# Optimization experiments

Hardware: AMD Instinct MI355X
Metric: run time of the kernel (lower is better)

Reference implementation:

```python
import jax, jax.numpy as jnp
import numpy as np
from jax import lax

THRESH = 1.0
MIN_VMEM = -1.0

def _conv(x, w, stride):
    # x: [N,C,H,W], w: [O,I,kh,kw]
    return lax.conv_general_dilated(
        x, w, window_strides=(stride, stride), padding=((1, 1), (1, 1)),
        dimension_numbers=("NCHW", "OIHW", "NCHW"))

def _avgpool2(x):
    n, c, h, w = x.shape
    return x.reshape(n, c, h // 2, 2, w // 2, 2).mean(axis=(3, 5))

def _iaf(x_bt, B, T):
    # x_bt: [B*T, ...] -> sinabs IAFSqueeze: reshape to [B,T,...], scan over T.
    feat = x_bt.shape[1:]
    seq = x_bt.reshape((B, T) + feat)
    seq_t = jnp.moveaxis(seq, 1, 0)  # [T, B, ...]

    def step(v, u):
        v = v + u                              # integrate
        s = (v >= THRESH).astype(v.dtype)      # SingleSpike
        v = v * (1.0 - s)                      # MembraneReset -> 0
        v = jnp.maximum(v, MIN_VMEM)           # min_v_mem clamp
        return v, s

    v0 = jnp.zeros(seq_t.shape[1:], dtype=x_bt.dtype)
    _, spikes = lax.scan(step, v0, seq_t)      # spikes: [T, B, ...]
    return jnp.moveaxis(spikes, 0, 1).reshape((B * T,) + feat)

def setup_inputs() -> dict:
    key = jax.random.key(0)
    k0, k1, k2, k3, k4 = jax.random.split(key, 5)
    x = jax.random.normal(k0, (25, 40, 2, 128, 128), jnp.float32)
    w1 = jax.random.normal(k1, (8, 2, 3, 3), jnp.float32) * 0.3
    w2 = jax.random.normal(k2, (16, 8, 3, 3), jnp.float32) * 0.2
    w3 = jax.random.normal(k3, (64, 1024), jnp.float32) * 0.1
    w4 = jax.random.normal(k4, (11, 64), jnp.float32) * 0.2
    return {"x": x, "w1": w1, "w2": w2, "w3": w3, "w4": w4}

def reference(x, w1, w2, w3, w4):
    B, T, C, H, W = x.shape
    h = x.reshape(B * T, C, H, W)
    h = _conv(h, w1, 2)          # [BT, 8, 64, 64]
    h = _iaf(h, B, T)
    h = _avgpool2(h)             # [BT, 8, 32, 32]
    h = _conv(h, w2, 2)          # [BT, 16, 16, 16]
    h = _iaf(h, B, T)
    h = _avgpool2(h)             # [BT, 16, 8, 8]
    h = h.reshape(B * T, -1)     # [BT, 1024]
    h = h @ w3.T                 # [BT, 64]
    h = _iaf(h, B, T)
    h = h @ w4.T                 # [BT, 11]
    h = _iaf(h, B, T)
    return h.reshape(B, T, -1)
```

## Files before the change

kernel.cpp:

```cpp
#include <hip/hip_runtime.h>

#define THRESH 1.0f
#define MIN_VMEM -1.0f

__device__ __forceinline__ float iaf_step(float& v, float u) {
    v += u;
    float s = (v >= THRESH) ? 1.f : 0.f;
    v = (s > 0.f) ? 0.f : v;
    v = fmaxf(v, MIN_VMEM);
    return s;
}

__global__ __launch_bounds__(64) void k1_conv1_iaf_pool(
        const float* __restrict__ x, const float* __restrict__ w1,
        float* __restrict__ ws1) {
    const int lane = threadIdx.x;
    const int q = blockIdx.x >> 1;
    const int g = blockIdx.x & 1;
    const int b = blockIdx.y;
    const bool q0 = (q == 0);

    float w[4][18];
    #pragma unroll
    for (int j = 0; j < 4; j++)
        #pragma unroll
        for (int k = 0; k < 18; k++)
            w[j][k] = w1[(4 * g + j) * 18 + k];

    const int iy0 = 4 * q - 1;
    int ro[5];
    #pragma unroll
    for (int r = 0; r < 5; r++) ro[r] = max(iy0 + r, 0) * 128;
    const float* xb = x + (size_t)(b * 40) * 32768 + 2 * lane;

    float2 A[10], Bv[10], N0[10], N1[10];
    #pragma unroll
    for (int ci = 0; ci < 2; ci++)
        #pragma unroll
        for (int r = 0; r < 5; r++) {
            A[ci * 5 + r]  = *(const float2*)(xb + ci * 16384 + ro[r]);
            Bv[ci * 5 + r] = *(const float2*)(xb + 32768 + ci * 16384 + ro[r]);
        }
    if (q0) {
        A[0] = make_float2(0.f, 0.f);  A[5] = make_float2(0.f, 0.f);
        Bv[0] = make_float2(0.f, 0.f); Bv[5] = make_float2(0.f, 0.f);
    }

    float vA[4], vB[4];
    #pragma unroll
    for (int j = 0; j < 4; j++) { vA[j] = 0.f; vB[j] = 0.f; }

    for (int tt = 0; tt < 20; tt++) {
        if (tt < 19) {
            const float* xn = xb + (size_t)(2 * tt + 2) * 32768;
            #pragma unroll
            for (int ci = 0; ci < 2; ci++)
                #pragma unroll
                for (int r = 0; r < 5; r++) {
                    N0[ci * 5 + r] = *(const float2*)(xn + ci * 16384 + ro[r]);
                    N1[ci * 5 + r] = *(const float2*)(xn + 32768 + ci * 16384 + ro[r]);
                }
        }
        #pragma unroll
        for (int half = 0; half < 2; half++) {
            const float2* F = half ? Bv : A;
            const int t = 2 * tt + half;
            float xm[10];
            #pragma unroll
            for (int r = 0; r < 10; r++) {
                const float up = __shfl_up(F[r].y, 1);
                xm[r] = (lane == 0) ? 0.f : up;
            }
            float preA[4], preB[4];
            #pragma unroll
            for (int j = 0; j < 4; j++) { preA[j] = 0.f; preB[j] = 0.f; }
            #pragma unroll
            for (int ci = 0; ci < 2; ci++)
                #pragma unroll
                for (int ky = 0; ky < 3; ky++) {
                    const int rA = ci * 5 + ky;
                    const int rB = rA + 2;
                    #pragma unroll
                    for (int j = 0; j < 4; j++) {
                        const float w0 = w[j][ci * 9 + ky * 3 + 0];
                        const float w1v = w[j][ci * 9 + ky * 3 + 1];
                        const float w2v = w[j][ci * 9 + ky * 3 + 2];
                        preA[j] += xm[rA] * w0 + F[rA].x * w1v + F[rA].y * w2v;
                        preB[j] += xm[rB] * w0 + F[rB].x * w1v + F[rB].y * w2v;
                    }
                }
            const size_t nbase = ((size_t)(b * 40 + t) * 8 + 4 * g) * 1024 + q * 32;
            #pragma unroll
            for (int j = 0; j < 4; j++) {
                float s = iaf_step(vA[j], preA[j]) + iaf_step(vB[j], preB[j]);
                s += __shfl_down(s, 1);
                if (!(lane & 1))
                    ws1[nbase + (size_t)j * 1024 + (lane >> 1)] = s * 0.25f;
            }
        }
        if (q0) {
            N0[0] = make_float2(0.f, 0.f); N0[5] = make_float2(0.f, 0.f);
            N1[0] = make_float2(0.f, 0.f); N1[5] = make_float2(0.f, 0.f);
        }
        #pragma unroll
        for (int r = 0; r < 10; r++) { A[r] = N0[r]; Bv[r] = N1[r]; }
    }
}

#define K2_CIS 1224

__global__ __launch_bounds__(256) void k2a_conv2(
        const float* __restrict__ ws1, const float* __restrict__ w2,
        float* __restrict__ u2) {
    __shared__ float F[8 * K2_CIS];
    const int n = blockIdx.x;
    const int tid = threadIdx.x;

    for (int i = tid; i < 8 * K2_CIS; i += 256) F[i] = 0.f;
    __syncthreads();
    const float4* src = (const float4*)(ws1 + (size_t)n * 8192);
    #pragma unroll
    for (int k = 0; k < 8; k++) {
        const int i = tid + 256 * k;
        const float4 q = src[i];
        const int ci = i >> 8;
        const int rr = i & 255;
        const int r = rr >> 3, c4 = rr & 7;
        float* d = &F[ci * K2_CIS + (r + 1) * 36 + 1 + 4 * c4];
        d[0] = q.x; d[1] = q.y; d[2] = q.z; d[3] = q.w;
    }
    __syncthreads();

    const int wv = tid >> 6;
    const int ln = tid & 63;
    const int oy = ln >> 2;
    const int ox4 = ln & 3;

    float acc[4][4];
    #pragma unroll
    for (int j = 0; j < 4; j++)
        #pragma unroll
        for (int k = 0; k < 4; k++) acc[j][k] = 0.f;

    #pragma unroll
    for (int ci = 0; ci < 8; ci++) {
        float q[3][9];
        const int base = ci * K2_CIS + (2 * oy) * 36 + 8 * ox4;
        #pragma unroll
        for (int ky = 0; ky < 3; ky++) {
            const float4 qa = *(const float4*)&F[base + ky * 36];
            const float4 qb = *(const float4*)&F[base + ky * 36 + 4];
            q[ky][0] = qa.x; q[ky][1] = qa.y; q[ky][2] = qa.z; q[ky][3] = qa.w;
            q[ky][4] = qb.x; q[ky][5] = qb.y; q[ky][6] = qb.z; q[ky][7] = qb.w;
            q[ky][8] = F[base + ky * 36 + 8];
        }
        #pragma unroll
        for (int j = 0; j < 4; j++) {
            const int co_u = __builtin_amdgcn_readfirstlane(4 * wv + j);
            const float* wb = w2 + co_u * 72 + ci * 9;
            float wm[9];
            #pragma unroll
            for (int m = 0; m < 9; m++) wm[m] = wb[m];
            #pragma unroll
            for (int k = 0; k < 4; k++)
                #pragma unroll
                for (int ky = 0; ky < 3; ky++)
                    #pragma unroll
                    for (int kx = 0; kx < 3; kx++)
                        acc[j][k] += q[ky][2 * k + kx] * wm[ky * 3 + kx];
        }
    }
    float* db = u2 + (size_t)n * 4096 + oy * 16 + 4 * ox4;
    #pragma unroll
    for (int j = 0; j < 4; j++) {
        const int co = 4 * wv + j;
        *(float4*)(db + co * 256) =
            make_float4(acc[j][0], acc[j][1], acc[j][2], acc[j][3]);
    }
}

__global__ __launch_bounds__(64) void k2b_scan(
        const float* __restrict__ u2, float* __restrict__ ws2) {
    const int id = blockIdx.x * 64 + threadIdx.x;
    const int b = id >> 10;
    const int c = (id >> 6) & 15;
    const int pp = id & 63;
    const int py = pp >> 3, px = pp & 7;
    const float* base = u2 + (size_t)(b * 40) * 4096 + c * 256
                      + (2 * py) * 16 + 2 * px;
    float* ob = ws2 + (size_t)(b * 40) * 1024 + c * 64 + py * 8 + px;

    float v0 = 0.f, v1 = 0.f, v2 = 0.f, v3 = 0.f;
    float2 P[2][8][2];
    #pragma unroll
    for (int tt = 0; tt < 8; tt++) {
        const float* nb = base + (size_t)tt * 4096;
        P[0][tt][0] = *(const float2*)(nb);
        P[0][tt][1] = *(const float2*)(nb + 16);
    }
    #pragma unroll
    for (int bt = 0; bt < 5; bt++) {
        if (bt < 4) {
            #pragma unroll
            for (int tt = 0; tt < 8; tt++) {
                const float* nb = base + (size_t)(8 * (bt + 1) + tt) * 4096;
                P[(bt + 1) & 1][tt][0] = *(const float2*)(nb);
                P[(bt + 1) & 1][tt][1] = *(const float2*)(nb + 16);
            }
        }
        #pragma unroll
        for (int tt = 0; tt < 8; tt++) {
            const float2 b0 = P[bt & 1][tt][0];
            const float2 b1 = P[bt & 1][tt][1];
            const float s = iaf_step(v0, b0.x) + iaf_step(v1, b0.y)
                          + iaf_step(v2, b1.x) + iaf_step(v3, b1.y);
            ob[(size_t)(8 * bt + tt) * 1024] = s * 0.25f;
        }
    }
}

__global__ __launch_bounds__(256) void k3_fc1(
        const float* __restrict__ ws2, const float* __restrict__ w3,
        float* __restrict__ ws3) {
    __shared__ float rows[2048];
    const int n0 = blockIdx.x * 2;
    const int tid = threadIdx.x;
    const float4* s = (const float4*)(ws2 + (size_t)n0 * 1024);
    #pragma unroll
    for (int k = 0; k < 2; k++)
        ((float4*)rows)[tid + 256 * k] = s[tid + 256 * k];
    __syncthreads();
    const int o = tid >> 2, ko = tid & 3;
    const float4* wp = (const float4*)(w3 + (size_t)o * 1024 + ko * 256);
    const float4* r0 = (const float4*)(rows + ko * 256);
    const float4* r1 = (const float4*)(rows + 1024 + ko * 256);
    float a0 = 0.f, a1 = 0.f;
    #pragma unroll 8
    for (int j = 0; j < 64; j++) {
        const float4 wv = wp[j];
        const float4 q0 = r0[j], q1 = r1[j];
        a0 += q0.x * wv.x + q0.y * wv.y + q0.z * wv.z + q0.w * wv.w;
        a1 += q1.x * wv.x + q1.y * wv.y + q1.z * wv.z + q1.w * wv.w;
    }
    a0 += __shfl_xor(a0, 1); a0 += __shfl_xor(a0, 2);
    a1 += __shfl_xor(a1, 1); a1 += __shfl_xor(a1, 2);
    if (ko == 0) {
        ws3[(size_t)(n0 + 0) * 64 + o] = a0;
        ws3[(size_t)(n0 + 1) * 64 + o] = a1;
    }
}

__global__ __launch_bounds__(256) void k4_iaf_fc2_iaf(
        const float* __restrict__ ws3, const float* __restrict__ w4,
        float* __restrict__ out) {
    __shared__ float sld[2560];
    __shared__ float pre[40 * 12];
    __shared__ float w4s[704];
    const int b = blockIdx.x, tid = threadIdx.x;

    const float4* src = (const float4*)(ws3 + (size_t)b * 2560);
    for (int i = tid; i < 640; i += 256) ((float4*)sld)[i] = src[i];
    for (int i = tid; i < 176; i += 256) ((float4*)w4s)[i] = ((const float4*)w4)[i];
    __syncthreads();
    if (tid < 64) {
        float v1 = 0.f;
        #pragma unroll
        for (int t = 0; t < 40; t++)
            sld[t * 64 + tid] = iaf_step(v1, sld[t * 64 + tid]);
    }
    __syncthreads();
    for (int idx = tid; idx < 440; idx += 256) {
        const int t = idx % 40, o = idx / 40;
        const float4* spr = (const float4*)(sld + t * 64);
        const float4* wr = (const float4*)(w4s + o * 64);
        float acc = 0.f;
        #pragma unroll
        for (int qq = 0; qq < 16; qq++) {
            const float4 a = spr[qq], ww = wr[qq];
            acc += a.x * ww.x + a.y * ww.y + a.z * ww.z + a.w * ww.w;
        }
        pre[t * 12 + o] = acc;
    }
    __syncthreads();
    if (tid < 11) {
        float v2 = 0.f;
        for (int t = 0; t < 40; t++)
            out[(size_t)(b * 40 + t) * 11 + tid] = iaf_step(v2, pre[t * 12 + tid]);
    }
}

extern "C" void kernel_launch(void* const* d_in, const int* in_sizes, int n_in,
                              void* d_out, int out_size, void* d_ws, size_t ws_size,
                              hipStream_t stream) {
    const float* x  = (const float*)d_in[0];
    const float* w1 = (const float*)d_in[1];
    const float* w2 = (const float*)d_in[2];
    const float* w3 = (const float*)d_in[3];
    const float* w4 = (const float*)d_in[4];
    float* out = (float*)d_out;

    float* ws1 = (float*)d_ws;
    float* ws2 = ws1 + 8192000;
    float* ws3 = ws2 + 1024000;
    float* u2 = (float*)d_in[0];

    k1_conv1_iaf_pool<<<dim3(64, 25), 64, 0, stream>>>(x, w1, ws1);
    k2a_conv2<<<1000, 256, 0, stream>>>(ws1, w2, u2);
    k2b_scan<<<400, 64, 0, stream>>>(u2, ws2);
    k3_fc1<<<500, 256, 0, stream>>>(ws2, w3, ws3);
    k4_iaf_fc2_iaf<<<25, 256, 0, stream>>>(ws3, w4, out);
}
```

Measured before the change: 267.0 us.

## Stage conv1 inputs through double-buffered LDS with async global-to-LDS loads

Replaces the register-held prefetch of two timesteps of input rows in the conv1+IAF+pool kernel with direct global-to-LDS loads (`global_load_lds`, 16 bytes per lane) into a two-slot LDS buffer. The next timestep's rows are loaded while the current one is computed, and the loop now steps one timestep at a time. The intent is to cut register pressure from the large float2 prefetch arrays and overlap memory with compute. In exchange it relies on hand-placed `vmcnt` waits that assume a fixed count of outstanding stores, and adds LDS reads per step.

```diff
diff --git a/kernel.cpp b/kernel.cpp
--- a/kernel.cpp
+++ b/kernel.cpp
@@ -11,9 +11,13 @@
     return s;
 }
 
+#define AS_G(p) ((const __attribute__((address_space(1))) void*)(p))
+#define AS_L(p) ((__attribute__((address_space(3))) void*)(p))
+
 __global__ __launch_bounds__(64) void k1_conv1_iaf_pool(
         const float* __restrict__ x, const float* __restrict__ w1,
         float* __restrict__ ws1) {
+    __shared__ float B[2][1280];
     const int lane = threadIdx.x;
     const int q = blockIdx.x >> 1;
     const int g = blockIdx.x & 1;
@@ -31,79 +35,84 @@
     int ro[5];
     #pragma unroll
     for (int r = 0; r < 5; r++) ro[r] = max(iy0 + r, 0) * 128;
-    const float* xb = x + (size_t)(b * 40) * 32768 + 2 * lane;
-
-    float2 A[10], Bv[10], N0[10], N1[10];
-    #pragma unroll
-    for (int ci = 0; ci < 2; ci++)
-        #pragma unroll
-        for (int r = 0; r < 5; r++) {
-            A[ci * 5 + r]  = *(const float2*)(xb + ci * 16384 + ro[r]);
-            Bv[ci * 5 + r] = *(const float2*)(xb + 32768 + ci * 16384 + ro[r]);
-        }
-    if (q0) {
-        A[0] = make_float2(0.f, 0.f);  A[5] = make_float2(0.f, 0.f);
-        Bv[0] = make_float2(0.f, 0.f); Bv[5] = make_float2(0.f, 0.f);
-    }
+    int goff[5];
+    #pragma unroll
+    for (int k = 0; k < 5; k++) {
+        const int m = 2 * k + (lane >> 5);
+        const int off = (m < 5) ? ro[m] : (16384 + ro[m - 5]);
+        goff[k] = off + (lane & 31) * 4;
+    }
+    const float* xb = x + (size_t)(b * 40) * 32768;
 
     float vA[4], vB[4];
     #pragma unroll
     for (int j = 0; j < 4; j++) { vA[j] = 0.f; vB[j] = 0.f; }
 
-    for (int tt = 0; tt < 20; tt++) {
-        if (tt < 19) {
-            const float* xn = xb + (size_t)(2 * tt + 2) * 32768;
-            #pragma unroll
-            for (int ci = 0; ci < 2; ci++)
+    {
+        #pragma unroll
+        for (int k = 0; k < 5; k++)
+            __builtin_amdgcn_global_load_lds(AS_G(xb + goff[k]),
+                                             AS_L(&B[0][k * 256]), 16, 0, 0);
+        asm volatile("s_waitcnt vmcnt(0)" ::: "memory");
+        if (q0) {
+            *(float2*)&B[0][2 * lane] = make_float2(0.f, 0.f);
+            *(float2*)&B[0][640 + 2 * lane] = make_float2(0.f, 0.f);
+        }
+    }
+
+    for (int t = 0; t < 40; t++) {
+        const int cur = t & 1;
+        const int nxt = cur ^ 1;
+        float2 F[10];
+        #pragma unroll
+        for (int m = 0; m < 10; m++)
+            F[m] = *(const float2*)&B[cur][m * 128 + 2 * lane];
+        if (t < 39) {
+            const float* xf = xb + (size_t)(t + 1) * 32768;
+            #pragma unroll
+            for (int k = 0; k < 5; k++)
+                __builtin_amdgcn_global_load_lds(AS_G(xf + goff[k]),
+                                                 AS_L(&B[nxt][k * 256]), 16, 0, 0);
+        }
+        float xm[10];
+        #pragma unroll
+        for (int r = 0; r < 10; r++) {
+            const float up = __shfl_up(F[r].y, 1);
+            xm[r] = (lane == 0) ? 0.f : up;
+        }
+        float preA[4], preB[4];
+        #pragma unroll
+        for (int j = 0; j < 4; j++) { preA[j] = 0.f; preB[j] = 0.f; }
+        #pragma unroll
+        for (int ci = 0; ci < 2; ci++)
+            #pragma unroll
+            for (int ky = 0; ky < 3; ky++) {
+                const int rA = ci * 5 + ky;
+                const int rB = rA + 2;
                 #pragma unroll
-                for (int r = 0; r < 5; r++) {
-                    N0[ci * 5 + r] = *(const float2*)(xn + ci * 16384 + ro[r]);
-                    N1[ci * 5 + r] = *(const float2*)(xn + 32768 + ci * 16384 + ro[r]);
+                for (int j = 0; j < 4; j++) {
+                    const float w0 = w[j][ci * 9 + ky * 3 + 0];
+                    const float w1v = w[j][ci * 9 + ky * 3 + 1];
+                    const float w2v = w[j][ci * 9 + ky * 3 + 2];
+                    preA[j] += xm[rA] * w0 + F[rA].x * w1v + F[rA].y * w2v;
+                    preB[j] += xm[rB] * w0 + F[rB].x * w1v + F[rB].y * w2v;
                 }
-        }
-        #pragma unroll
-        for (int half = 0; half < 2; half++) {
-            const float2* F = half ? Bv : A;
-            const int t = 2 * tt + half;
-            float xm[10];
-            #pragma unroll
-            for (int r = 0; r < 10; r++) {
-                const float up = __shfl_up(F[r].y, 1);
-                xm[r] = (lane == 0) ? 0.f : up;
             }
-            float preA[4], preB[4];
-            #pragma unroll
-            for (int j = 0; j < 4; j++) { preA[j] = 0.f; preB[j] = 0.f; }
-            #pragma unroll
-            for (int ci = 0; ci < 2; ci++)
-                #pragma unroll
-                for (int ky = 0; ky < 3; ky++) {
-                    const int rA = ci * 5 + ky;
-                    const int rB = rA + 2;
-                    #pragma unroll
-                    for (int j = 0; j < 4; j++) {
-                        const float w0 = w[j][ci * 9 + ky * 3 + 0];
-                        const float w1v = w[j][ci * 9 + ky * 3 + 1];
-                        const float w2v = w[j][ci * 9 + ky * 3 + 2];
-                        preA[j] += xm[rA] * w0 + F[rA].x * w1v + F[rA].y * w2v;
-                        preB[j] += xm[rB] * w0 + F[rB].x * w1v + F[rB].y * w2v;
-                    }
-                }
-            const size_t nbase = ((size_t)(b * 40 + t) * 8 + 4 * g) * 1024 + q * 32;
-            #pragma unroll
-            for (int j = 0; j < 4; j++) {
-                float s = iaf_step(vA[j], preA[j]) + iaf_step(vB[j], preB[j]);
-                s += __shfl_down(s, 1);
-                if (!(lane & 1))
-                    ws1[nbase + (size_t)j * 1024 + (lane >> 1)] = s * 0.25f;
+        const size_t nbase = ((size_t)(b * 40 + t) * 8 + 4 * g) * 1024 + q * 32;
+        #pragma unroll
+        for (int j = 0; j < 4; j++) {
+            float s = iaf_step(vA[j], preA[j]) + iaf_step(vB[j], preB[j]);
+            s += __shfl_down(s, 1);
+            if (!(lane & 1))
+                ws1[nbase + (size_t)j * 1024 + (lane >> 1)] = s * 0.25f;
+        }
+        if (t < 39) {
+            asm volatile("s_waitcnt vmcnt(4)" ::: "memory");
+            if (q0) {
+                *(float2*)&B[nxt][2 * lane] = make_float2(0.f, 0.f);
+                *(float2*)&B[nxt][640 + 2 * lane] = make_float2(0.f, 0.f);
             }
         }
-        if (q0) {
-            N0[0] = make_float2(0.f, 0.f); N0[5] = make_float2(0.f, 0.f);
-            N1[0] = make_float2(0.f, 0.f); N1[5] = make_float2(0.f, 0.f);
-        }
-        #pragma unroll
-        for (int r = 0; r < 10; r++) { A[r] = N0[r]; Bv[r] = N1[r]; }
     }
 }
 
```

After: 264.4 us. No clear change (-1.0%).

## Stage conv1 input tiles in shared memory and split channels across warps

Applied to the files above, without the earlier changes.

The conv1+IAF+pool kernel now runs 128-thread blocks that cooperatively load four timesteps of input rows into shared memory with float4 loads. Each thread then computes a 2x2 pooled output patch for two output channels, reading its neighbours from LDS instead of using shuffles. Each block covers all 8 channels, so the input is no longer read twice by two channel-group blocks. The cost is a barrier per chunk, fewer blocks in the grid (800), and the loss of the register prefetch of the next timestep.

```diff
diff --git a/kernel.cpp b/kernel.cpp
--- a/kernel.cpp
+++ b/kernel.cpp
@@ -11,99 +11,109 @@
     return s;
 }
 
-__global__ __launch_bounds__(64) void k1_conv1_iaf_pool(
+__global__ __launch_bounds__(128) void k1_conv1_iaf_pool(
         const float* __restrict__ x, const float* __restrict__ w1,
         float* __restrict__ ws1) {
-    const int lane = threadIdx.x;
-    const int q = blockIdx.x >> 1;
-    const int g = blockIdx.x & 1;
+    __shared__ float S[5120];
+    const int tid = threadIdx.x;
+    const int cog = tid >> 5;
+    const int pc = tid & 31;
+    const int q = blockIdx.x;
     const int b = blockIdx.y;
     const bool q0 = (q == 0);
 
-    float w[4][18];
-    #pragma unroll
-    for (int j = 0; j < 4; j++)
+    float w[2][18];
+    #pragma unroll
+    for (int j = 0; j < 2; j++)
         #pragma unroll
         for (int k = 0; k < 18; k++)
-            w[j][k] = w1[(4 * g + j) * 18 + k];
-
-    const int iy0 = 4 * q - 1;
-    int ro[5];
-    #pragma unroll
-    for (int r = 0; r < 5; r++) ro[r] = max(iy0 + r, 0) * 128;
-    const float* xb = x + (size_t)(b * 40) * 32768 + 2 * lane;
-
-    float2 A[10], Bv[10], N0[10], N1[10];
-    #pragma unroll
-    for (int ci = 0; ci < 2; ci++)
-        #pragma unroll
-        for (int r = 0; r < 5; r++) {
-            A[ci * 5 + r]  = *(const float2*)(xb + ci * 16384 + ro[r]);
-            Bv[ci * 5 + r] = *(const float2*)(xb + 32768 + ci * 16384 + ro[r]);
-        }
-    if (q0) {
-        A[0] = make_float2(0.f, 0.f);  A[5] = make_float2(0.f, 0.f);
-        Bv[0] = make_float2(0.f, 0.f); Bv[5] = make_float2(0.f, 0.f);
-    }
-
-    float vA[4], vB[4];
-    #pragma unroll
-    for (int j = 0; j < 4; j++) { vA[j] = 0.f; vB[j] = 0.f; }
-
-    for (int tt = 0; tt < 20; tt++) {
-        if (tt < 19) {
-            const float* xn = xb + (size_t)(2 * tt + 2) * 32768;
-            #pragma unroll
-            for (int ci = 0; ci < 2; ci++)
-                #pragma unroll
-                for (int r = 0; r < 5; r++) {
-                    N0[ci * 5 + r] = *(const float2*)(xn + ci * 16384 + ro[r]);
-                    N1[ci * 5 + r] = *(const float2*)(xn + 32768 + ci * 16384 + ro[r]);
+            w[j][k] = w1[(cog + 4 * j) * 18 + k];
+
+    int gofs[10];
+    #pragma unroll
+    for (int k = 0; k < 10; k++) {
+        const int i = tid + 128 * k;
+        const int t = i / 320;
+        const int rem = i - 320 * t;
+        const int ci = rem / 160;
+        const int rr = (rem - 160 * ci) >> 5;
+        const int f4 = rem & 31;
+        const int grow = max(4 * q - 1 + rr, 0);
+        gofs[k] = t * 32768 + ci * 16384 + grow * 128 + 4 * f4;
+    }
+
+    float v[2][4];
+    #pragma unroll
+    for (int j = 0; j < 2; j++)
+        #pragma unroll
+        for (int s4 = 0; s4 < 4; s4++) v[j][s4] = 0.f;
+
+    const float* xb = x + (size_t)(b * 40) * 32768;
+
+    for (int ch = 0; ch < 10; ch++) {
+        const int t0 = ch * 4;
+        __syncthreads();
+        const float* xc = xb + (size_t)t0 * 32768;
+        #pragma unroll
+        for (int k = 0; k < 10; k++)
+            *(float4*)&S[4 * (tid + 128 * k)] = *(const float4*)(xc + gofs[k]);
+        if (q0) {
+            #pragma unroll
+            for (int m = 0; m < 8; m++) {
+                const int i2 = tid + 128 * m;
+                const int t = i2 >> 8;
+                const int ci = (i2 >> 7) & 1;
+                const int c = i2 & 127;
+                S[((t * 2 + ci) * 5) * 128 + c] = 0.f;
+            }
+        }
+        __syncthreads();
+        #pragma unroll
+        for (int tc = 0; tc < 4; tc++) {
+            float pre[2][4];
+            #pragma unroll
+            for (int j = 0; j < 2; j++)
+                #pragma unroll
+                for (int o = 0; o < 4; o++) pre[j][o] = 0.f;
+            #pragma unroll
+            for (int ci = 0; ci < 2; ci++) {
+                float p[5][5];
+                #pragma unroll
+                for (int dy = 0; dy < 5; dy++) {
+                    const int rowoff = ((tc * 2 + ci) * 5 + dy) * 128;
+                    const float4 a = *(const float4*)&S[rowoff + 4 * pc];
+                    float lv = S[rowoff + (pc ? 4 * pc - 1 : 0)];
+                    lv = pc ? lv : 0.f;
+                    p[dy][0] = lv;
+                    p[dy][1] = a.x; p[dy][2] = a.y;
+                    p[dy][3] = a.z; p[dy][4] = a.w;
                 }
-        }
-        #pragma unroll
-        for (int half = 0; half < 2; half++) {
-            const float2* F = half ? Bv : A;
-            const int t = 2 * tt + half;
-            float xm[10];
-            #pragma unroll
-            for (int r = 0; r < 10; r++) {
-                const float up = __shfl_up(F[r].y, 1);
-                xm[r] = (lane == 0) ? 0.f : up;
+                #pragma unroll
+                for (int j = 0; j < 2; j++)
+                    #pragma unroll
+                    for (int ry = 0; ry < 2; ry++)
+                        #pragma unroll
+                        for (int cx = 0; cx < 2; cx++) {
+                            float acc = pre[j][ry * 2 + cx];
+                            #pragma unroll
+                            for (int ky = 0; ky < 3; ky++)
+                                #pragma unroll
+                                for (int kx = 0; kx < 3; kx++)
+                                    acc += p[2 * ry + ky][2 * cx + kx]
+                                         * w[j][ci * 9 + ky * 3 + kx];
+                            pre[j][ry * 2 + cx] = acc;
+                        }
             }
-            float preA[4], preB[4];
-            #pragma unroll
-            for (int j = 0; j < 4; j++) { preA[j] = 0.f; preB[j] = 0.f; }
-            #pragma unroll
-            for (int ci = 0; ci < 2; ci++)
-                #pragma unroll
-                for (int ky = 0; ky < 3; ky++) {
-                    const int rA = ci * 5 + ky;
-                    const int rB = rA + 2;
-                    #pragma unroll
-                    for (int j = 0; j < 4; j++) {
-                        const float w0 = w[j][ci * 9 + ky * 3 + 0];
-                        const float w1v = w[j][ci * 9 + ky * 3 + 1];
-                        const float w2v = w[j][ci * 9 + ky * 3 + 2];
-                        preA[j] += xm[rA] * w0 + F[rA].x * w1v + F[rA].y * w2v;
-                        preB[j] += xm[rB] * w0 + F[rB].x * w1v + F[rB].y * w2v;
-                    }
-                }
-            const size_t nbase = ((size_t)(b * 40 + t) * 8 + 4 * g) * 1024 + q * 32;
-            #pragma unroll
-            for (int j = 0; j < 4; j++) {
-                float s = iaf_step(vA[j], preA[j]) + iaf_step(vB[j], preB[j]);
-                s += __shfl_down(s, 1);
-                if (!(lane & 1))
-                    ws1[nbase + (size_t)j * 1024 + (lane >> 1)] = s * 0.25f;
+            const size_t nbase = (size_t)(b * 40 + t0 + tc) * 8192 + q * 32 + pc;
+            #pragma unroll
+            for (int j = 0; j < 2; j++) {
+                float s = 0.f;
+                #pragma unroll
+                for (int o = 0; o < 4; o++)
+                    s += iaf_step(v[j][o], pre[j][o]);
+                ws1[nbase + (size_t)(cog + 4 * j) * 1024] = s * 0.25f;
             }
         }
-        if (q0) {
-            N0[0] = make_float2(0.f, 0.f); N0[5] = make_float2(0.f, 0.f);
-            N1[0] = make_float2(0.f, 0.f); N1[5] = make_float2(0.f, 0.f);
-        }
-        #pragma unroll
-        for (int r = 0; r < 10; r++) { A[r] = N0[r]; Bv[r] = N1[r]; }
     }
 }
 
@@ -304,7 +314,7 @@
     float* ws3 = ws2 + 1024000;
     float* u2 = (float*)d_in[0];
 
-    k1_conv1_iaf_pool<<<dim3(64, 25), 64, 0, stream>>>(x, w1, ws1);
+    k1_conv1_iaf_pool<<<dim3(32, 25), 128, 0, stream>>>(x, w1, ws1);
     k2a_conv2<<<1000, 256, 0, stream>>>(ws1, w2, u2);
     k2b_scan<<<400, 64, 0, stream>>>(u2, ws2);
     k3_fc1<<<500, 256, 0, stream>>>(ws2, w3, ws3);
```

Result: slower. 361.2 us (+35.3%).
